# Kernel optimization log

Hardware: AMD Instinct MI355X
Metric: run time of the kernel (lower is better)

The kernel has to match this reference:

```python
import jax, jax.numpy as jnp
import numpy as np

N = 50000
E = 800000
H1 = 4
CIN = 256
COUT = 64
NC = 16
HID = H1 * COUT  # 256


def _glorot(key, shape):
    fan_in, fan_out = shape[-1], shape[-2]
    s = float(np.sqrt(6.0 / (fan_in + fan_out)))
    return jax.random.uniform(key, shape, jnp.float32, -s, s)


def setup_inputs() -> dict:
    key = jax.random.key(0)
    ks = jax.random.split(key, 12)
    x = jax.random.normal(ks[0], (N, CIN), jnp.float32)
    edge_index = jax.random.randint(ks[1], (2, E), 0, N, jnp.int64)
    # layer 1 params (H1 heads, concat)
    W1 = _glorot(ks[2], (H1, COUT, CIN))
    b1 = jnp.zeros((H1, COUT), jnp.float32)
    a11_w = _glorot(ks[3], (H1, 1, COUT)).reshape(H1, COUT)
    a11_b = jnp.zeros((H1,), jnp.float32)
    a12_w = _glorot(ks[4], (H1, 1, COUT)).reshape(H1, COUT)
    a12_b = jnp.zeros((H1,), jnp.float32)
    bias1 = jnp.zeros((HID,), jnp.float32)
    # layer 2 params (1 head, mean)
    W2 = _glorot(ks[5], (1, NC, HID))
    b2 = jnp.zeros((1, NC), jnp.float32)
    a21_w = _glorot(ks[6], (1, 1, NC)).reshape(1, NC)
    a21_b = jnp.zeros((1,), jnp.float32)
    a22_w = _glorot(ks[7], (1, 1, NC)).reshape(1, NC)
    a22_b = jnp.zeros((1,), jnp.float32)
    bias2 = jnp.zeros((NC,), jnp.float32)
    return dict(x=x, edge_index=edge_index, W1=W1, b1=b1, a11_w=a11_w, a11_b=a11_b,
                a12_w=a12_w, a12_b=a12_b, bias1=bias1, W2=W2, b2=b2,
                a21_w=a21_w, a21_b=a21_b, a22_w=a22_w, a22_b=a22_b, bias2=bias2)


def _gat_layer(x, src, dst, W, b, a1w, a1b, a2w, a2b, lbias, concat):
    n = x.shape[0]
    h = jnp.einsum('ni,hoi->nho', x, W) + b            # [N,H,O]
    s1 = jnp.einsum('nho,ho->nh', h, a1w) + a1b        # per-node head score (source side)
    s2 = jnp.einsum('nho,ho->nh', h, a2w) + a2b        # per-node head score (target side)
    e = s2[dst] + s1[src]                              # [E,H]
    e = jnp.where(e > 0, e, 0.2 * e)                   # LeakyReLU(0.2)
    m = jax.ops.segment_max(e, dst, num_segments=n)
    ex = jnp.exp(e - m[dst])
    den = jax.ops.segment_sum(ex, dst, num_segments=n)
    att = ex / (den[dst] + 1e-16)                      # segment softmax over incoming edges
    msg = h[src] * att[..., None]                      # [E,H,O]
    if concat:
        msg = msg.reshape(msg.shape[0], -1)            # [E,H*O]
    else:
        msg = msg.mean(axis=1)                         # [E,O]
    out = jax.ops.segment_sum(msg, dst, num_segments=n)
    return out + lbias


def reference(x, edge_index, W1, b1, a11_w, a11_b, a12_w, a12_b, bias1,
              W2, b2, a21_w, a21_b, a22_w, a22_b, bias2):
    n = x.shape[0]
    loops = jnp.arange(n, dtype=edge_index.dtype)
    src = jnp.concatenate([edge_index[0], loops])
    dst = jnp.concatenate([edge_index[1], loops])
    # eval mode: dropout is identity
    h = _gat_layer(x, src, dst, W1, b1, a11_w, a11_b, a12_w, a12_b, bias1, concat=True)
    h = jax.nn.elu(h)
    out = _gat_layer(h, src, dst, W2, b2, a21_w, a21_b, a22_w, a22_b, bias2, concat=False)
    return jax.nn.log_softmax(out, axis=1)
```

## Files before the change

### kernel.cpp

```cpp
#include <hip/hip_runtime.h>
#include <math.h>

constexpr int NN  = 50000;
constexpr int NE  = 800000;
constexpr int NT  = NE + NN;
constexpr int CI  = 256;
constexpr int HIDn = 256;
constexpr int NCn = 16;
constexpr int NPAD = 50048;
constexpr int CVTB = 32;
constexpr float SOFF = 16.f;

constexpr int NB    = 196;
constexpr int EPBA  = 4096;
constexpr int NBLKA = (NT + EPBA - 1) / EPBA;
constexpr int CAPB  = 6144;

typedef __attribute__((ext_vector_type(8))) short bf16x8;
typedef __attribute__((ext_vector_type(4))) float f32x4;

__device__ __forceinline__ float lrelu(float x){ return x > 0.f ? x : 0.2f*x; }

__device__ __forceinline__ unsigned short f2b(float f) {
    union { float f; unsigned u; } v; v.f = f;
    unsigned u = v.u;
    return (unsigned short)((u + 0x7FFFu + ((u >> 16) & 1u)) >> 16);
}
__device__ __forceinline__ float b2f(unsigned short b) {
    union { unsigned u; float f; } v; v.u = (unsigned)b << 16;
    return v.f;
}

__device__ __forceinline__ void edge_sd(const int* __restrict__ ei, int e, int& s, int& d) {
    if (e < NE) { s = ei[e]; d = ei[NE + e]; }
    else { s = e - NE; d = s; }
}

__global__ __launch_bounds__(256) void k_hist(const float* __restrict__ W1,
        unsigned short* __restrict__ wb, const int* __restrict__ ei,
        int* __restrict__ bcnt) {
    int b = blockIdx.x, t = threadIdx.x;
    if (b < CVTB) {
        int i = b * 256 + t;
        const float4* p = reinterpret_cast<const float4*>(W1) + (size_t)i * 2;
        float4 a = p[0], bb = p[1];
        bf16x8 r;
        r[0] = (short)f2b(a.x);  r[1] = (short)f2b(a.y);
        r[2] = (short)f2b(a.z);  r[3] = (short)f2b(a.w);
        r[4] = (short)f2b(bb.x); r[5] = (short)f2b(bb.y);
        r[6] = (short)f2b(bb.z); r[7] = (short)f2b(bb.w);
        *(reinterpret_cast<bf16x8*>(wb) + i) = r;
        return;
    }
    __shared__ int hist[NB];
    int blk = b - CVTB;
    if (t < NB) hist[t] = 0;
    __syncthreads();
    int e0 = blk * EPBA;
    #pragma unroll
    for (int i = 0; i < 16; ++i) {
        int e = e0 + i * 256 + t;
        if (e < NT) {
            int s, d; edge_sd(ei, e, s, d);
            atomicAdd(&hist[d >> 8], 1);
        }
    }
    __syncthreads();
    if (t < NB && hist[t] > 0) atomicAdd(&bcnt[t], hist[t]);
}

__global__ __launch_bounds__(256) void k_scanB(const int* __restrict__ bcnt,
        int* __restrict__ boff, int* __restrict__ bcur, int* __restrict__ row_off) {
    __shared__ int tmp[256];
    int t = threadIdx.x;
    int v = (t < NB) ? bcnt[t] : 0;
    tmp[t] = v;
    __syncthreads();
    #pragma unroll
    for (int off = 1; off < 256; off <<= 1) {
        int u = (t >= off) ? tmp[t - off] : 0;
        __syncthreads();
        tmp[t] += u;
        __syncthreads();
    }
    int ex = tmp[t] - v;
    if (t < NB) { boff[t] = ex; bcur[t] = ex; }
    if (t == NB - 1) boff[NB] = ex + v;
    if (t == 0) row_off[NN] = NT;
}

__global__ __launch_bounds__(256) void k_binA(const int* __restrict__ ei,
        int* __restrict__ bcur, unsigned* __restrict__ part_arr) {
    __shared__ unsigned vload[EPBA];
    __shared__ unsigned short rload[EPBA];
    __shared__ unsigned char  bload[EPBA];
    __shared__ unsigned sorted[EPBA];
    __shared__ unsigned char  bsort[EPBA];
    __shared__ int hist[NB], lbase[NB], gbase[NB], tmp[256];
    int t = threadIdx.x, blk = blockIdx.x;
    int e0 = blk * EPBA;
    int cnt = min(EPBA, NT - e0);
    if (t < NB) hist[t] = 0;
    __syncthreads();
    for (int slot = t; slot < cnt; slot += 256) {
        int e = e0 + slot;
        int s, d; edge_sd(ei, e, s, d);
        int bb = d >> 8;
        vload[slot] = (unsigned)s | ((unsigned)(d & 255) << 16);
        bload[slot] = (unsigned char)bb;
        rload[slot] = (unsigned short)atomicAdd(&hist[bb], 1);
    }
    __syncthreads();
    tmp[t] = (t < NB) ? hist[t] : 0;
    __syncthreads();
    #pragma unroll
    for (int off = 1; off < 256; off <<= 1) {
        int u = (t >= off) ? tmp[t - off] : 0;
        __syncthreads();
        tmp[t] += u;
        __syncthreads();
    }
    if (t < NB) lbase[t] = tmp[t] - hist[t];
    __syncthreads();
    if (t < NB && hist[t] > 0) gbase[t] = atomicAdd(&bcur[t], hist[t]);
    __syncthreads();
    for (int p = t; p < cnt; p += 256) {
        int bb = bload[p];
        int q = lbase[bb] + rload[p];
        sorted[q] = vload[p];
        bsort[q] = (unsigned char)bb;
    }
    __syncthreads();
    for (int q = t; q < cnt; q += 256) {
        int bb = bsort[q];
        part_arr[gbase[bb] + (q - lbase[bb])] = sorted[q];
    }
}

__global__ __launch_bounds__(256) void k_binB(const unsigned* __restrict__ part_arr,
        const int* __restrict__ boff, int* __restrict__ row_off,
        int* __restrict__ csr_src) {
    __shared__ int hist[256], loff[256], tmp[256];
    __shared__ int stage[CAPB];
    __shared__ unsigned short rr[CAPB];
    int b = blockIdx.x, t = threadIdx.x;
    int bb = boff[b], cnt = boff[b + 1] - bb;
    hist[t] = 0;
    __syncthreads();
    if (cnt <= CAPB) {
        for (int p = t; p < cnt; p += 256) {
            unsigned v = part_arr[bb + p];
            rr[p] = (unsigned short)atomicAdd(&hist[v >> 16], 1);
        }
        __syncthreads();
        tmp[t] = hist[t];
        __syncthreads();
        #pragma unroll
        for (int off = 1; off < 256; off <<= 1) {
            int u = (t >= off) ? tmp[t - off] : 0;
            __syncthreads();
            tmp[t] += u;
            __syncthreads();
        }
        loff[t] = tmp[t] - hist[t];
        int node = b * 256 + t;
        if (node < NN) row_off[node] = bb + loff[t];
        __syncthreads();
        for (int p = t; p < cnt; p += 256) {
            unsigned v = part_arr[bb + p];
            stage[loff[v >> 16] + rr[p]] = (int)(v & 0xFFFFu);
        }
        __syncthreads();
        for (int p = t; p < cnt; p += 256) csr_src[bb + p] = stage[p];
    }
}

__global__ __launch_bounds__(256) void k_gemm1m(const float* __restrict__ x,
        const unsigned short* __restrict__ wb, const float* __restrict__ b1,
        const float* __restrict__ a11w, const float* __restrict__ a11b,
        const float* __restrict__ a12w, const float* __restrict__ a12b,
        unsigned short* __restrict__ h1b, float* __restrict__ s11, float* __restrict__ s12) {
    __shared__ unsigned short xs[64 * 256];
    int tid = threadIdx.x;
    int wv = tid >> 6, lane = tid & 63;
    int n0 = blockIdx.x * 64;

    {
        char* ls = (char*)xs;
        const float* xblk = x + (size_t)n0 * CI;
        #pragma unroll
        for (int c = 0; c < 8; ++c) {
            int idx = c * 256 + tid;
            int row = idx >> 5;
            int n = n0 + row;
            bf16x8 r = {};
            if (n < NN) {
                const float4* fp = reinterpret_cast<const float4*>(xblk + (size_t)idx * 8);
                float4 a = fp[0], b = fp[1];
                r[0] = (short)f2b(a.x); r[1] = (short)f2b(a.y);
                r[2] = (short)f2b(a.z); r[3] = (short)f2b(a.w);
                r[4] = (short)f2b(b.x); r[5] = (short)f2b(b.y);
                r[6] = (short)f2b(b.z); r[7] = (short)f2b(b.w);
            }
            int G = idx * 16;
            int Ldst = G ^ (((G >> 9) & 7) << 4);
            *(bf16x8*)(ls + Ldst) = r;
        }
    }
    __syncthreads();

    int rsel = lane & 15, ksel = lane >> 4;
    f32x4 acc[4][4] = {};
    const char* ls = (const char*)xs;
    const unsigned short* wbase = wb + (size_t)(wv * 64 + rsel) * CI + ksel * 8;
    #pragma unroll
    for (int kk = 0; kk < 8; ++kk) {
        bf16x8 a[4], b[4];
        #pragma unroll
        for (int r = 0; r < 4; ++r) {
            int row = r * 16 + rsel;
            int T = row * 512 + kk * 64 + ksel * 16;
            a[r] = *(const bf16x8*)(ls + (T ^ ((row & 7) << 4)));
        }
        #pragma unroll
        for (int c = 0; c < 4; ++c)
            b[c] = *(const bf16x8*)(wbase + (size_t)c * 16 * CI + kk * 32);
        #pragma unroll
        for (int r = 0; r < 4; ++r)
            #pragma unroll
            for (int c = 0; c < 4; ++c)
                acc[r][c] = __builtin_amdgcn_mfma_f32_16x16x32_bf16(a[r], b[c], acc[r][c], 0, 0, 0);
    }

    float bbc[4], aw1c[4], aw2c[4];
    #pragma unroll
    for (int c = 0; c < 4; ++c) {
        int col = wv * 64 + c * 16 + rsel;
        bbc[c] = b1[col]; aw1c[c] = a11w[col]; aw2c[c] = a12w[col];
    }
    float ab1 = a11b[wv], ab2 = a12b[wv];
    #pragma unroll
    for (int r = 0; r < 4; ++r) {
        #pragma unroll
        for (int j = 0; j < 4; ++j) {
            int n = n0 + r * 16 + ksel * 4 + j;
            float p1 = 0.f, p2 = 0.f;
            #pragma unroll
            for (int c = 0; c < 4; ++c) {
                float v = acc[r][c][j] + bbc[c];
                if (n < NN) h1b[(size_t)n * HIDn + wv * 64 + c * 16 + rsel] = f2b(v);
                p1 = fmaf(v, aw1c[c], p1);
                p2 = fmaf(v, aw2c[c], p2);
            }
            #pragma unroll
            for (int o = 1; o < 16; o <<= 1) {
                p1 += __shfl_xor(p1, o, 16);
                p2 += __shfl_xor(p2, o, 16);
            }
            if (rsel == 0 && n < NN) {
                s11[n * 4 + wv] = p1 + ab1;
                s12[n * 4 + wv] = p2 + ab2;
            }
        }
    }
}

__global__ __launch_bounds__(256) void k_node1f(const int* __restrict__ row_off,
        const int* __restrict__ csr_src, const float* __restrict__ s11,
        const float* __restrict__ s12, const unsigned short* __restrict__ h1b,
        const float* __restrict__ bias1, unsigned short* __restrict__ out1b) {
    int lane = threadIdx.x & 63;
    int d = blockIdx.x * 4 + (threadIdx.x >> 6);
    int beg = row_off[d], endo = row_off[d + 1];
    int eo = lane >> 2, h = lane & 3;
    float s2v = s12[d * 4 + h];
    float l = 0.f;
    for (int k0 = beg; k0 < endo; k0 += 16) {
        int k = k0 + eo;
        if (k < endo)
            l += __expf(lrelu(s11[csr_src[k] * 4 + h] + s2v) - SOFF);
    }
    #pragma unroll
    for (int o = 4; o < 64; o <<= 1) l += __shfl_xor(l, o);
    int h2 = lane >> 4;
    float sh  = __shfl(s2v, h2);
    float inv = 1.f / (__shfl(l, h2) + 1e-30f);
    float ax0 = 0.f, ay0 = 0.f, az0 = 0.f, aw0 = 0.f;
    float ax1 = 0.f, ay1 = 0.f, az1 = 0.f, aw1 = 0.f;
    int hi = lane & 48;
    for (int k0 = beg; k0 < endo; k0 += 16) {
        int kw = k0 + (lane & 15);
        float wv = 0.f; int sw = 0;
        if (kw < endo) {
            sw = csr_src[kw];
            wv = __expf(lrelu(s11[sw * 4 + h2] + sh) - SOFF) * inv;
        }
        int lim = min(16, endo - k0);
        int e = 0;
        for (; e + 2 <= lim; e += 2) {
            float w0 = __shfl(wv, e + hi),     w1 = __shfl(wv, e + 1 + hi);
            int   s0 = __shfl(sw, e + hi),     s1 = __shfl(sw, e + 1 + hi);
            ushort4 r0 = *(reinterpret_cast<const ushort4*>(h1b + (size_t)s0 * HIDn) + lane);
            ushort4 r1 = *(reinterpret_cast<const ushort4*>(h1b + (size_t)s1 * HIDn) + lane);
            ax0 = fmaf(w0, b2f(r0.x), ax0); ay0 = fmaf(w0, b2f(r0.y), ay0);
            az0 = fmaf(w0, b2f(r0.z), az0); aw0 = fmaf(w0, b2f(r0.w), aw0);
            ax1 = fmaf(w1, b2f(r1.x), ax1); ay1 = fmaf(w1, b2f(r1.y), ay1);
            az1 = fmaf(w1, b2f(r1.z), az1); aw1 = fmaf(w1, b2f(r1.w), aw1);
        }
        if (e < lim) {
            float w0 = __shfl(wv, e + hi);
            int   s0 = __shfl(sw, e + hi);
            ushort4 r0 = *(reinterpret_cast<const ushort4*>(h1b + (size_t)s0 * HIDn) + lane);
            ax0 = fmaf(w0, b2f(r0.x), ax0); ay0 = fmaf(w0, b2f(r0.y), ay0);
            az0 = fmaf(w0, b2f(r0.z), az0); aw0 = fmaf(w0, b2f(r0.w), aw0);
        }
    }
    int f0 = lane * 4;
    float4 bb = *reinterpret_cast<const float4*>(bias1 + f0);
    float v0 = ax0 + ax1 + bb.x, v1 = ay0 + ay1 + bb.y;
    float v2 = az0 + az1 + bb.z, v3 = aw0 + aw1 + bb.w;
    v0 = v0 > 0.f ? v0 : __expf(v0) - 1.f;
    v1 = v1 > 0.f ? v1 : __expf(v1) - 1.f;
    v2 = v2 > 0.f ? v2 : __expf(v2) - 1.f;
    v3 = v3 > 0.f ? v3 : __expf(v3) - 1.f;
    ushort4 o;
    o.x = f2b(v0); o.y = f2b(v1); o.z = f2b(v2); o.w = f2b(v3);
    *(reinterpret_cast<ushort4*>(out1b + (size_t)d * HIDn) + lane) = o;
}

__global__ __launch_bounds__(256) void k_gemm2s(const unsigned short* __restrict__ hid,
        const float* __restrict__ W2, const float* __restrict__ b2,
        const float* __restrict__ a21w, const float* __restrict__ a21b,
        const float* __restrict__ a22w, const float* __restrict__ a22b,
        unsigned short* __restrict__ z2b, float* __restrict__ s21, float* __restrict__ s22) {
    __shared__ float ws[16][260];
    int t = threadIdx.x;
    {
        int r = t >> 4, c0 = (t & 15) * 16;
        const float4* src = reinterpret_cast<const float4*>(W2 + r * 256 + c0);
        #pragma unroll
        for (int q = 0; q < 4; ++q)
            *reinterpret_cast<float4*>(&ws[r][c0 + q * 4]) = src[q];
    }
    __syncthreads();
    int c = t & 15;
    int n = blockIdx.x * 16 + (t >> 4);
    if (n >= NN) return;
    const bf16x8* hp = reinterpret_cast<const bf16x8*>(hid + (size_t)n * HIDn);
    float acc = 0.f;
    #pragma unroll 8
    for (int i = 0; i < HIDn / 8; ++i) {
        bf16x8 hv = hp[i];
        #pragma unroll
        for (int j = 0; j < 8; ++j)
            acc = fmaf(b2f((unsigned short)hv[j]), ws[c][i * 8 + j], acc);
    }
    float v = acc + b2[c];
    z2b[(size_t)n * NCn + c] = f2b(v);
    float p1 = v * a21w[c], p2 = v * a22w[c];
    #pragma unroll
    for (int o = 1; o < 16; o <<= 1) {
        p1 += __shfl_xor(p1, o, 16);
        p2 += __shfl_xor(p2, o, 16);
    }
    if (c == 0) { s21[n] = p1 + a21b[0]; s22[n] = p2 + a22b[0]; }
}

__global__ __launch_bounds__(256) void k_node2f(const int* __restrict__ row_off,
        const int* __restrict__ csr_src, const float* __restrict__ s21,
        const float* __restrict__ s22, const unsigned short* __restrict__ z2b,
        const float* __restrict__ bias2, float* __restrict__ out) {
    int lane = threadIdx.x & 63;
    int d = blockIdx.x * 4 + (threadIdx.x >> 6);
    int beg = row_off[d], endo = row_off[d + 1];
    float s2v = s22[d];
    float l = 0.f;
    for (int k0 = beg; k0 < endo; k0 += 64) {
        int k = k0 + lane;
        if (k < endo)
            l += __expf(lrelu(s21[csr_src[k]] + s2v) - SOFF);
    }
    #pragma unroll
    for (int o = 1; o < 64; o <<= 1) l += __shfl_xor(l, o);
    float inv = 1.f / (l + 1e-30f);
    int e4 = lane >> 4, c = lane & 15;
    float acc = 0.f;
    for (int k0 = beg; k0 < endo; k0 += 64) {
        int kw = k0 + lane;
        float wv = 0.f; int sw = 0;
        if (kw < endo) {
            sw = csr_src[kw];
            wv = __expf(lrelu(s21[sw] + s2v) - SOFF) * inv;
        }
        int lim = min(64, endo - k0);
        for (int e0 = 0; e0 < lim; e0 += 4) {
            int e = e0 + e4;
            float w = __shfl(wv, e);
            int   s = __shfl(sw, e);
            acc = fmaf(w, b2f(z2b[(size_t)s * NCn + c]), acc);
        }
    }
    acc += __shfl_xor(acc, 16);
    acc += __shfl_xor(acc, 32);
    float v = acc + bias2[c];
    float mx = v;
    #pragma unroll
    for (int o = 1; o < 16; o <<= 1) mx = fmaxf(mx, __shfl_xor(mx, o, 16));
    float sm = __expf(v - mx);
    #pragma unroll
    for (int o = 1; o < 16; o <<= 1) sm += __shfl_xor(sm, o, 16);
    if (lane < 16) out[(size_t)d * NCn + c] = v - mx - logf(sm);
}

extern "C" void kernel_launch(void* const* d_in, const int* in_sizes, int n_in,
                              void* d_out, int out_size, void* d_ws, size_t ws_size,
                              hipStream_t stream) {
    const float* x     = (const float*)d_in[0];
    const int*   ei    = (const int*)d_in[1];
    const float* W1    = (const float*)d_in[2];
    const float* b1    = (const float*)d_in[3];
    const float* a11w  = (const float*)d_in[4];
    const float* a11b  = (const float*)d_in[5];
    const float* a12w  = (const float*)d_in[6];
    const float* a12b  = (const float*)d_in[7];
    const float* bias1 = (const float*)d_in[8];
    const float* W2    = (const float*)d_in[9];
    const float* b2    = (const float*)d_in[10];
    const float* a21w  = (const float*)d_in[11];
    const float* a21b  = (const float*)d_in[12];
    const float* a22w  = (const float*)d_in[13];
    const float* a22b  = (const float*)d_in[14];
    const float* bias2 = (const float*)d_in[15];
    float* out = (float*)d_out;

    char* w = (char*)d_ws;
    unsigned short* wb    = (unsigned short*)w; w += (size_t)HIDn * CI * 2;
    unsigned short* h1b   = (unsigned short*)w; w += (size_t)NN * HIDn * 2;
    unsigned short* out1b = (unsigned short*)w; w += (size_t)NN * HIDn * 2;
    unsigned short* z2b   = (unsigned short*)w; w += (size_t)NN * NCn * 2;
    int*      csr_src  = (int*)w;      w += (size_t)NT * 4;
    unsigned* part_arr = (unsigned*)w; w += (size_t)NT * 4;
    float* s11     = (float*)w; w += (size_t)NN * 4 * 4;
    float* s12     = (float*)w; w += (size_t)NN * 4 * 4;
    float* s21     = (float*)w; w += (size_t)NN * 4;
    float* s22     = (float*)w; w += (size_t)NN * 4;
    int*   row_off = (int*)w;   w += (size_t)(NN + 1) * 4;
    int*   bcnt    = (int*)w;   w += (size_t)(NB + 1) * 4;
    int*   boff    = (int*)w;   w += (size_t)(NB + 1) * 4;
    int*   bcur    = (int*)w;   w += (size_t)(NB + 1) * 4;

    hipMemsetAsync(bcnt, 0, (size_t)(NB + 1) * 4, stream);

    k_hist<<<CVTB + NBLKA, 256, 0, stream>>>(W1, wb, ei, bcnt);

    k_gemm1m<<<NPAD / 64, 256, 0, stream>>>(x, wb, b1, a11w, a11b, a12w, a12b,
                                            h1b, s11, s12);

    k_scanB<<<1, 256, 0, stream>>>(bcnt, boff, bcur, row_off);
    k_binA<<<NBLKA, 256, 0, stream>>>(ei, bcur, part_arr);
    k_binB<<<NB, 256, 0, stream>>>(part_arr, boff, row_off, csr_src);

    k_node1f<<<NN / 4, 256, 0, stream>>>(row_off, csr_src, s11, s12, h1b, bias1, out1b);

    k_gemm2s<<<(NN + 15) / 16, 256, 0, stream>>>(out1b, W2, b2, a21w, a21b, a22w, a22b,
                                                 z2b, s21, s22);
    k_node2f<<<NN / 4, 256, 0, stream>>>(row_off, csr_src, s21, s22, z2b, bias2, out);
}
```

Baseline: 201.8 us.

## Cache attention exponentials in LDS and unroll neighbour gathers in GAT aggregation

```diff
diff --git a/kernel.cpp b/kernel.cpp
--- a/kernel.cpp
+++ b/kernel.cpp
@@ -15,6 +15,7 @@
 constexpr int EPBA  = 4096;
 constexpr int NBLKA = (NT + EPBA - 1) / EPBA;
 constexpr int CAPB  = 6144;
+constexpr int MAXCH = 8;
 
 typedef __attribute__((ext_vector_type(8))) short bf16x8;
 typedef __attribute__((ext_vector_type(4))) float f32x4;
@@ -269,56 +270,70 @@
         const int* __restrict__ csr_src, const float* __restrict__ s11,
         const float* __restrict__ s12, const unsigned short* __restrict__ h1b,
         const float* __restrict__ bias1, unsigned short* __restrict__ out1b) {
-    int lane = threadIdx.x & 63;
-    int d = blockIdx.x * 4 + (threadIdx.x >> 6);
+    __shared__ float wlds[4][MAXCH * 64];
+    int tid = threadIdx.x;
+    int lane = tid & 63, w2 = tid >> 6;
+    int d = blockIdx.x * 4 + w2;
     int beg = row_off[d], endo = row_off[d + 1];
+    int nch = (endo - beg + 15) >> 4;
     int eo = lane >> 2, h = lane & 3;
     float s2v = s12[d * 4 + h];
     float l = 0.f;
-    for (int k0 = beg; k0 < endo; k0 += 16) {
-        int k = k0 + eo;
+    for (int c = 0; c < nch; ++c) {
+        int k = beg + c * 16 + eo;
+        float ex = 0.f;
         if (k < endo)
-            l += __expf(lrelu(s11[csr_src[k] * 4 + h] + s2v) - SOFF);
+            ex = __expf(lrelu(s11[csr_src[k] * 4 + h] + s2v) - SOFF);
+        if (c < MAXCH) wlds[w2][c * 64 + lane] = ex;
+        l += ex;
     }
     #pragma unroll
     for (int o = 4; o < 64; o <<= 1) l += __shfl_xor(l, o);
     int h2 = lane >> 4;
     float sh  = __shfl(s2v, h2);
     float inv = 1.f / (__shfl(l, h2) + 1e-30f);
-    float ax0 = 0.f, ay0 = 0.f, az0 = 0.f, aw0 = 0.f;
-    float ax1 = 0.f, ay1 = 0.f, az1 = 0.f, aw1 = 0.f;
+    int tr = (lane & 15) * 4 + h2;
     int hi = lane & 48;
-    for (int k0 = beg; k0 < endo; k0 += 16) {
+    float a0x=0.f,a0y=0.f,a0z=0.f,a0w=0.f, a1x=0.f,a1y=0.f,a1z=0.f,a1w=0.f;
+    float a2x=0.f,a2y=0.f,a2z=0.f,a2w=0.f, a3x=0.f,a3y=0.f,a3z=0.f,a3w=0.f;
+    for (int c = 0; c < nch; ++c) {
+        int k0 = beg + c * 16;
         int kw = k0 + (lane & 15);
-        float wv = 0.f; int sw = 0;
-        if (kw < endo) {
-            sw = csr_src[kw];
-            wv = __expf(lrelu(s11[sw * 4 + h2] + sh) - SOFF) * inv;
+        int sw = 0;
+        if (kw < endo) sw = csr_src[kw];
+        float wv;
+        if (c < MAXCH) {
+            wv = wlds[w2][c * 64 + tr] * inv;
+        } else {
+            wv = 0.f;
+            if (kw < endo) wv = __expf(lrelu(s11[sw * 4 + h2] + sh) - SOFF) * inv;
         }
         int lim = min(16, endo - k0);
-        int e = 0;
-        for (; e + 2 <= lim; e += 2) {
+        for (int e = 0; e < lim; e += 4) {
             float w0 = __shfl(wv, e + hi),     w1 = __shfl(wv, e + 1 + hi);
+            float w2f = __shfl(wv, e + 2 + hi), w3 = __shfl(wv, e + 3 + hi);
             int   s0 = __shfl(sw, e + hi),     s1 = __shfl(sw, e + 1 + hi);
+            int   s2 = __shfl(sw, e + 2 + hi), s3 = __shfl(sw, e + 3 + hi);
             ushort4 r0 = *(reinterpret_cast<const ushort4*>(h1b + (size_t)s0 * HIDn) + lane);
             ushort4 r1 = *(reinterpret_cast<const ushort4*>(h1b + (size_t)s1 * HIDn) + lane);
-            ax0 = fmaf(w0, b2f(r0.x), ax0); ay0 = fmaf(w0, b2f(r0.y), ay0);
-            az0 = fmaf(w0, b2f(r0.z), az0); aw0 = fmaf(w0, b2f(r0.w), aw0);
-            ax1 = fmaf(w1, b2f(r1.x), ax1); ay1 = fmaf(w1, b2f(r1.y), ay1);
-            az1 = fmaf(w1, b2f(r1.z), az1); aw1 = fmaf(w1, b2f(r1.w), aw1);
-        }
-        if (e < lim) {
-            float w0 = __shfl(wv, e + hi);
-            int   s0 = __shfl(sw, e + hi);
-            ushort4 r0 = *(reinterpret_cast<const ushort4*>(h1b + (size_t)s0 * HIDn) + lane);
-            ax0 = fmaf(w0, b2f(r0.x), ax0); ay0 = fmaf(w0, b2f(r0.y), ay0);
-            az0 = fmaf(w0, b2f(r0.z), az0); aw0 = fmaf(w0, b2f(r0.w), aw0);
+            ushort4 r2 = *(reinterpret_cast<const ushort4*>(h1b + (size_t)s2 * HIDn) + lane);
+            ushort4 r3 = *(reinterpret_cast<const ushort4*>(h1b + (size_t)s3 * HIDn) + lane);
+            a0x = fmaf(w0, b2f(r0.x), a0x); a0y = fmaf(w0, b2f(r0.y), a0y);
+            a0z = fmaf(w0, b2f(r0.z), a0z); a0w = fmaf(w0, b2f(r0.w), a0w);
+            a1x = fmaf(w1, b2f(r1.x), a1x); a1y = fmaf(w1, b2f(r1.y), a1y);
+            a1z = fmaf(w1, b2f(r1.z), a1z); a1w = fmaf(w1, b2f(r1.w), a1w);
+            a2x = fmaf(w2f, b2f(r2.x), a2x); a2y = fmaf(w2f, b2f(r2.y), a2y);
+            a2z = fmaf(w2f, b2f(r2.z), a2z); a2w = fmaf(w2f, b2f(r2.w), a2w);
+            a3x = fmaf(w3, b2f(r3.x), a3x); a3y = fmaf(w3, b2f(r3.y), a3y);
+            a3z = fmaf(w3, b2f(r3.z), a3z); a3w = fmaf(w3, b2f(r3.w), a3w);
         }
     }
     int f0 = lane * 4;
     float4 bb = *reinterpret_cast<const float4*>(bias1 + f0);
-    float v0 = ax0 + ax1 + bb.x, v1 = ay0 + ay1 + bb.y;
-    float v2 = az0 + az1 + bb.z, v3 = aw0 + aw1 + bb.w;
+    float v0 = a0x + a1x + a2x + a3x + bb.x;
+    float v1 = a0y + a1y + a2y + a3y + bb.y;
+    float v2 = a0z + a1z + a2z + a3z + bb.z;
+    float v3 = a0w + a1w + a2w + a3w + bb.w;
     v0 = v0 > 0.f ? v0 : __expf(v0) - 1.f;
     v1 = v1 > 0.f ? v1 : __expf(v1) - 1.f;
     v2 = v2 > 0.f ? v2 : __expf(v2) - 1.f;
@@ -373,31 +388,51 @@
     int lane = threadIdx.x & 63;
     int d = blockIdx.x * 4 + (threadIdx.x >> 6);
     int beg = row_off[d], endo = row_off[d + 1];
+    int deg = endo - beg;
     float s2v = s22[d];
-    float l = 0.f;
-    for (int k0 = beg; k0 < endo; k0 += 64) {
-        int k = k0 + lane;
-        if (k < endo)
-            l += __expf(lrelu(s21[csr_src[k]] + s2v) - SOFF);
-    }
-    #pragma unroll
-    for (int o = 1; o < 64; o <<= 1) l += __shfl_xor(l, o);
-    float inv = 1.f / (l + 1e-30f);
     int e4 = lane >> 4, c = lane & 15;
     float acc = 0.f;
-    for (int k0 = beg; k0 < endo; k0 += 64) {
-        int kw = k0 + lane;
-        float wv = 0.f; int sw = 0;
-        if (kw < endo) {
-            sw = csr_src[kw];
-            wv = __expf(lrelu(s21[sw] + s2v) - SOFF) * inv;
-        }
-        int lim = min(64, endo - k0);
-        for (int e0 = 0; e0 < lim; e0 += 4) {
+    if (deg <= 64) {
+        int k = beg + lane;
+        float exr = 0.f; int swr = 0;
+        if (k < endo) {
+            swr = csr_src[k];
+            exr = __expf(lrelu(s21[swr] + s2v) - SOFF);
+        }
+        float l = exr;
+        #pragma unroll
+        for (int o = 1; o < 64; o <<= 1) l += __shfl_xor(l, o);
+        float wv = exr / (l + 1e-30f);
+        for (int e0 = 0; e0 < deg; e0 += 4) {
             int e = e0 + e4;
             float w = __shfl(wv, e);
-            int   s = __shfl(sw, e);
+            int   s = __shfl(swr, e);
             acc = fmaf(w, b2f(z2b[(size_t)s * NCn + c]), acc);
+        }
+    } else {
+        float l = 0.f;
+        for (int k0 = beg; k0 < endo; k0 += 64) {
+            int k = k0 + lane;
+            if (k < endo)
+                l += __expf(lrelu(s21[csr_src[k]] + s2v) - SOFF);
+        }
+        #pragma unroll
+        for (int o = 1; o < 64; o <<= 1) l += __shfl_xor(l, o);
+        float inv = 1.f / (l + 1e-30f);
+        for (int k0 = beg; k0 < endo; k0 += 64) {
+            int kw = k0 + lane;
+            float wv = 0.f; int sw = 0;
+            if (kw < endo) {
+                sw = csr_src[kw];
+                wv = __expf(lrelu(s21[sw] + s2v) - SOFF) * inv;
+            }
+            int lim = min(64, endo - k0);
+            for (int e0 = 0; e0 < lim; e0 += 4) {
+                int e = e0 + e4;
+                float w = __shfl(wv, e);
+                int   s = __shfl(sw, e);
+                acc = fmaf(w, b2f(z2b[(size_t)s * NCn + c]), acc);
+            }
         }
     }
     acc += __shfl_xor(acc, 16);
```

New measurement: 196.3 us. 1.03x faster.
